# Kernel tuning notes

Hardware: AMD Instinct MI355X
Metric: run time of the kernel (lower is better)

Reference implementation:

```python
import jax, jax.numpy as jnp
import numpy as np

N_NODES = 100000
N_EDGES = 1600000
IN_FEAT = 128
EMBED = 64
N_LAYERS = 3
N_CENTROID = 100
N_CLASS = 10
EPS = 1e-12


def setup_inputs() -> dict:
    key = jax.random.key(0)
    ks = jax.random.split(key, 8)
    x = jax.random.normal(ks[0], (N_NODES, IN_FEAT), dtype=jnp.float32)
    edge_index = jax.random.randint(ks[1], (2, N_EDGES), 0, N_NODES, dtype=jnp.int64)
    W_embed = jax.random.normal(ks[2], (EMBED, IN_FEAT), dtype=jnp.float32) / np.sqrt(IN_FEAT)
    W_gcn = jax.random.normal(ks[3], (N_LAYERS, EMBED, EMBED), dtype=jnp.float32) / np.sqrt(EMBED)
    b_gcn = jnp.zeros((N_LAYERS, EMBED), dtype=jnp.float32)
    centroids = jax.random.normal(ks[4], (N_CENTROID, EMBED), dtype=jnp.float32)
    W_out = jax.random.normal(ks[5], (N_CLASS, N_CENTROID), dtype=jnp.float32) / np.sqrt(N_CENTROID)
    b_out = jnp.zeros((N_CLASS,), dtype=jnp.float32)
    return {"x": x, "edge_index": edge_index, "W_embed": W_embed, "W_gcn": W_gcn,
            "b_gcn": b_gcn, "centroids": centroids, "W_out": W_out, "b_out": b_out}


def _gcn_norm(edge_index, n, dtype):
    # add self loops, compute symmetric D^{-1/2}(A+I)D^{-1/2} edge weights
    loops = jnp.arange(n, dtype=edge_index.dtype)
    src = jnp.concatenate([edge_index[0], loops])
    dst = jnp.concatenate([edge_index[1], loops])
    deg = jax.ops.segment_sum(jnp.ones_like(dst, dtype=dtype), dst, num_segments=n)
    dinv = jax.lax.rsqrt(jnp.maximum(deg, 1.0))
    norm = dinv[src] * dinv[dst]  # [E+N]
    return src, dst, norm


def reference(x, edge_index, W_embed, W_gcn, b_gcn, centroids, W_out, b_out):
    n = x.shape[0]
    src, dst, norm = _gcn_norm(edge_index, n, x.dtype)
    # Euclidean manifold: log/exp are identity
    h = x @ W_embed.T  # [N, D]
    for l in range(W_gcn.shape[0]):
        hw = h @ W_gcn[l].T                                   # [N, D]
        msg = hw[src] * norm[:, None]                         # gather  [E+N, D]
        h = jax.ops.segment_sum(msg, dst, num_segments=n)     # scatter [N, D]
        h = jax.nn.relu(h + b_gcn[l])
    # centroid distances: ||h_i - c_k|| via expanded quadratic (avoids [N,K,D])
    h2 = jnp.sum(h * h, axis=-1, keepdims=True)               # [N, 1]
    c2 = jnp.sum(centroids * centroids, axis=-1)[None, :]     # [1, K]
    d2 = jnp.maximum(h2 + c2 - 2.0 * (h @ centroids.T), 0.0)  # [N, K]
    dist = jnp.sqrt(d2 + EPS)
    pooled = dist.mean(axis=0)                                # [K] graph pooling
    return pooled @ W_out.T + b_out                           # [num_class]
```

## Files before the change

### kernel.cpp

```cpp
#include <hip/hip_runtime.h>
#include <hip/hip_bf16.h>

typedef unsigned int uint32;
typedef float floatx2 __attribute__((ext_vector_type(2)));
typedef __attribute__((ext_vector_type(8))) short bf16x8;
typedef __attribute__((ext_vector_type(4))) float f32x4;

#define CHUNK 16384


__global__ __launch_bounds__(256) void k_bhist(const int* __restrict__ dst,
                                               int* __restrict__ bcnt,
                                               int E, int NBUCK, int NCH) {
    __shared__ int h[512];
    int c = blockIdx.x, tid = threadIdx.x;
    for (int i = tid; i < NBUCK; i += 256) h[i] = 0;
    __syncthreads();
    int base = c * CHUNK;
#pragma unroll
    for (int k = 0; k < CHUNK / 256; ++k) {
        int e = base + k * 256 + tid;
        if (e < E) atomicAdd(&h[dst[e] >> 8], 1);
    }
    __syncthreads();
    for (int i = tid; i < NBUCK; i += 256) bcnt[(size_t)i * NCH + c] = h[i];
}

__global__ __launch_bounds__(128) void k_bscan1(const int* __restrict__ bcnt,
                                                int* __restrict__ bofs,
                                                int* __restrict__ btot, int NCH) {
    __shared__ int tmp[128];
    int b = blockIdx.x, t = threadIdx.x;
    int v = (t < NCH) ? bcnt[(size_t)b * NCH + t] : 0;
    tmp[t] = v;
    __syncthreads();
    for (int off = 1; off < 128; off <<= 1) {
        int u = (t >= off) ? tmp[t - off] : 0;
        __syncthreads();
        tmp[t] += u;
        __syncthreads();
    }
    if (t < NCH) bofs[(size_t)b * NCH + t] = tmp[t] - v;
    if (t == 127) btot[b] = tmp[127];
}

__global__ __launch_bounds__(512) void k_bscan2(const int* __restrict__ btot,
                                                int* __restrict__ bbase, int nb) {
    __shared__ int tmp[512];
    int t = threadIdx.x;
    int v = (t < nb) ? btot[t] : 0;
    tmp[t] = v;
    __syncthreads();
    for (int off = 1; off < 512; off <<= 1) {
        int u = (t >= off) ? tmp[t - off] : 0;
        __syncthreads();
        tmp[t] += u;
        __syncthreads();
    }
    if (t < nb) bbase[t] = tmp[t] - v;
    if (t == nb - 1) bbase[nb] = tmp[t];
}

__global__ __launch_bounds__(256) void k_bscatter(const int* __restrict__ ei,
                                                  const int* __restrict__ bbase,
                                                  const int* __restrict__ bofs,
                                                  uint32* __restrict__ ebuf,
                                                  int E, int NBUCK, int NCH) {
    __shared__ int cur[512];
    int c = blockIdx.x, tid = threadIdx.x;
    for (int i = tid; i < NBUCK; i += 256)
        cur[i] = bbase[i] + bofs[(size_t)i * NCH + c];
    __syncthreads();
    int base = c * CHUNK;
#pragma unroll
    for (int k = 0; k < CHUNK / 256; ++k) {
        int e = base + k * 256 + tid;
        if (e < E) {
            int s = ei[e];
            int d = ei[E + e];
            int p = atomicAdd(&cur[d >> 8], 1);
            ebuf[p] = (uint32)s | ((uint32)(d & 255) << 20);
        }
    }
}

__global__ __launch_bounds__(256) void k_bsort(const uint32* __restrict__ ebuf,
                                               const int* __restrict__ bbase,
                                               int* __restrict__ ssrc,
                                               int2* __restrict__ rc,
                                               float* __restrict__ dinv, int N) {
    __shared__ int h[256];
    __shared__ int sc[256];
    __shared__ int cur[256];
    int b = blockIdx.x, tid = threadIdx.x;
    int beg = bbase[b], end = bbase[b + 1];
    h[tid] = 0;
    __syncthreads();
    for (int j = beg + tid; j < end; j += 256)
        atomicAdd(&h[(ebuf[j] >> 20) & 255], 1);
    __syncthreads();
    int v = h[tid];
    sc[tid] = v;
    __syncthreads();
    for (int off = 1; off < 256; off <<= 1) {
        int u = (tid >= off) ? sc[tid - off] : 0;
        __syncthreads();
        sc[tid] += u;
        __syncthreads();
    }
    int rowbase = beg + sc[tid] - v;
    cur[tid] = rowbase;
    int d = b * 256 + tid;
    if (d < N) {
        rc[d] = make_int2(rowbase, v);
        dinv[d] = rsqrtf((float)(v + 1));
    }
    __syncthreads();
    for (int j = beg + tid; j < end; j += 256) {
        uint32 w = ebuf[j];
        int p = atomicAdd(&cur[(w >> 20) & 255], 1);
        ssrc[p] = (int)(w & 0xFFFFFu);
    }
}


__device__ __forceinline__ short f2bf(float f) {
    __hip_bfloat16 b = __float2bfloat16(f);
    return __builtin_bit_cast(short, b);
}

__device__ __forceinline__ bf16x8 pack_bf16x8(float4 v0, float4 v1) {
    bf16x8 r;
    r[0] = f2bf(v0.x); r[1] = f2bf(v0.y); r[2] = f2bf(v0.z); r[3] = f2bf(v0.w);
    r[4] = f2bf(v1.x); r[5] = f2bf(v1.y); r[6] = f2bf(v1.z); r[7] = f2bf(v1.w);
    return r;
}


__global__ __launch_bounds__(256) void k_embed(const float* __restrict__ x,
                                               const float* __restrict__ We,
                                               float* __restrict__ h, int N) {
    int lane = threadIdx.x & 63;
    int w = threadIdx.x >> 6;
    int l15 = lane & 15;
    int lg = lane >> 4;

    bf16x8 B[4][4];
#pragma unroll
    for (int ct = 0; ct < 4; ++ct) {
        const float* wr = We + (size_t)(ct * 16 + l15) * 128 + lg * 8;
#pragma unroll
        for (int ks = 0; ks < 4; ++ks) {
            float4 v0 = *(const float4*)(wr + ks * 32);
            float4 v1 = *(const float4*)(wr + ks * 32 + 4);
            B[ct][ks] = pack_bf16x8(v0, v1);
        }
    }

    int rowbase = blockIdx.x * 256 + w * 64;

    f32x4 acc[4][4];
#pragma unroll
    for (int rt = 0; rt < 4; ++rt)
#pragma unroll
        for (int ct = 0; ct < 4; ++ct)
            acc[rt][ct] = (f32x4){0.f, 0.f, 0.f, 0.f};

#pragma unroll
    for (int ks = 0; ks < 4; ++ks) {
#pragma unroll
        for (int rt = 0; rt < 4; ++rt) {
            int row = rowbase + rt * 16 + l15;
            row = (row < N) ? row : (N - 1);
            const float* xr = x + (size_t)row * 128 + ks * 32 + lg * 8;
            float4 v0 = *(const float4*)xr;
            float4 v1 = *(const float4*)(xr + 4);
            bf16x8 a = pack_bf16x8(v0, v1);
#pragma unroll
            for (int ct = 0; ct < 4; ++ct)
                acc[rt][ct] = __builtin_amdgcn_mfma_f32_16x16x32_bf16(
                    a, B[ct][ks], acc[rt][ct], 0, 0, 0);
        }
    }

#pragma unroll
    for (int rt = 0; rt < 4; ++rt) {
        int row0 = rowbase + rt * 16 + lg * 4;
#pragma unroll
        for (int r = 0; r < 4; ++r) {
            int row = row0 + r;
            if (row < N) {
#pragma unroll
                for (int ct = 0; ct < 4; ++ct)
                    h[(size_t)row * 64 + ct * 16 + l15] = acc[rt][ct][r];
            }
        }
    }
}


__global__ __launch_bounds__(256) void k_gcn(const float* __restrict__ hin,
                                             const float* __restrict__ Wg,
                                             const float* __restrict__ bias_prev, int act,
                                             const float* __restrict__ dinv,
                                             uint32* __restrict__ tab, int N) {
    int lane = threadIdx.x & 63;
    int w = threadIdx.x >> 6;
    int l15 = lane & 15, lg = lane >> 4;

    bf16x8 A[4][2];
#pragma unroll
    for (int rt = 0; rt < 4; ++rt) {
        const float* wr = Wg + (size_t)(rt * 16 + l15) * 64 + lg * 8;
#pragma unroll
        for (int ks = 0; ks < 2; ++ks) {
            float4 v0 = *(const float4*)(wr + ks * 32);
            float4 v1 = *(const float4*)(wr + ks * 32 + 4);
            A[rt][ks] = pack_bf16x8(v0, v1);
        }
    }

    float bv[16];
#pragma unroll
    for (int ks = 0; ks < 2; ++ks) {
        float4 b0 = *(const float4*)(bias_prev + ks * 32 + lg * 8);
        float4 b1 = *(const float4*)(bias_prev + ks * 32 + lg * 8 + 4);
        bv[ks * 8 + 0] = b0.x; bv[ks * 8 + 1] = b0.y;
        bv[ks * 8 + 2] = b0.z; bv[ks * 8 + 3] = b0.w;
        bv[ks * 8 + 4] = b1.x; bv[ks * 8 + 5] = b1.y;
        bv[ks * 8 + 6] = b1.z; bv[ks * 8 + 7] = b1.w;
    }

    int nodebase = blockIdx.x * 256 + w * 64;

#pragma unroll
    for (int nt = 0; nt < 4; ++nt) {
        int node = nodebase + nt * 16 + l15;
        int nodec = (node < N) ? node : (N - 1);
        const float* hr = hin + ((size_t)nodec << 6) + lg * 8;

        bf16x8 Bf[2];
#pragma unroll
        for (int ks = 0; ks < 2; ++ks) {
            float4 v0 = *(const float4*)(hr + ks * 32);
            float4 v1 = *(const float4*)(hr + ks * 32 + 4);
            if (act) {
                v0.x = fmaxf(v0.x + bv[ks * 8 + 0], 0.f);
                v0.y = fmaxf(v0.y + bv[ks * 8 + 1], 0.f);
                v0.z = fmaxf(v0.z + bv[ks * 8 + 2], 0.f);
                v0.w = fmaxf(v0.w + bv[ks * 8 + 3], 0.f);
                v1.x = fmaxf(v1.x + bv[ks * 8 + 4], 0.f);
                v1.y = fmaxf(v1.y + bv[ks * 8 + 5], 0.f);
                v1.z = fmaxf(v1.z + bv[ks * 8 + 6], 0.f);
                v1.w = fmaxf(v1.w + bv[ks * 8 + 7], 0.f);
            }
            Bf[ks] = pack_bf16x8(v0, v1);
        }

        f32x4 acc[4];
#pragma unroll
        for (int rt = 0; rt < 4; ++rt) acc[rt] = (f32x4){0.f, 0.f, 0.f, 0.f};
#pragma unroll
        for (int ks = 0; ks < 2; ++ks)
#pragma unroll
            for (int rt = 0; rt < 4; ++rt)
                acc[rt] = __builtin_amdgcn_mfma_f32_16x16x32_bf16(
                    A[rt][ks], Bf[ks], acc[rt], 0, 0, 0);

        float s = dinv[nodec];
        if (node < N) {
#pragma unroll
            for (int rt = 0; rt < 4; ++rt) {
                int u = 0;
                u = __builtin_amdgcn_cvt_pk_fp8_f32(acc[rt][0] * s, acc[rt][1] * s, u, false);
                u = __builtin_amdgcn_cvt_pk_fp8_f32(acc[rt][2] * s, acc[rt][3] * s, u, true);
                tab[(size_t)node * 16 + rt * 4 + lg] = u;
            }
        }
    }
}


__global__ __launch_bounds__(256) void k_agg(const int2* __restrict__ rc,
                                             const int* __restrict__ ssrc,
                                             const float* __restrict__ dinv,
                                             const uint2* __restrict__ tab2,
                                             float* __restrict__ out, int N) {
    int lane = threadIdx.x & 63;
    int d = blockIdx.x * 4 + (threadIdx.x >> 6);
    if (d >= N) return;
    int q = lane & 7;
    int sub = lane >> 3;
    int l15 = lane & 15;
    int hi = lane & 48;

    floatx2 a01 = {0.f, 0.f}, a23 = {0.f, 0.f}, a45 = {0.f, 0.f}, a67 = {0.f, 0.f};
    auto accum = [&](uint2 v) {
        a01 += __builtin_amdgcn_cvt_pk_f32_fp8((int)v.x, false);
        a23 += __builtin_amdgcn_cvt_pk_f32_fp8((int)v.x, true);
        a45 += __builtin_amdgcn_cvt_pk_f32_fp8((int)v.y, false);
        a67 += __builtin_amdgcn_cvt_pk_f32_fp8((int)v.y, true);
    };

    {
        uint2 v = tab2[(size_t)d * 8 + q];
        if (sub == 0) accum(v);
    }

    int2 r = rc[d];
    int beg = __builtin_amdgcn_readfirstlane(r.x);
    int cnt = __builtin_amdgcn_readfirstlane(r.y);
    const int* srow = ssrc + beg;

    int j = 0;
    for (; j + 16 <= cnt; j += 16) {
        int ev = srow[j + l15];
        int t0 = __shfl(ev, hi | sub);
        int t1 = __shfl(ev, hi | 8 | sub);
        uint2 v0 = tab2[(size_t)t0 * 8 + q];
        uint2 v1 = tab2[(size_t)t1 * 8 + q];
        accum(v0);
        accum(v1);
    }
    int rem = cnt - j;
    if (rem) {
        int ev = srow[j + l15];
        int t0 = __shfl(ev, hi | sub);
        int t1 = __shfl(ev, hi | 8 | sub);
        t0 = (sub < rem) ? t0 : N;
        t1 = (sub + 8 < rem) ? t1 : N;
        uint2 v0 = tab2[(size_t)t0 * 8 + q];
        uint2 v1 = tab2[(size_t)t1 * 8 + q];
        accum(v0);
        accum(v1);
    }

    float a[8] = {a01.x, a01.y, a23.x, a23.y, a45.x, a45.y, a67.x, a67.y};
#pragma unroll
    for (int i = 0; i < 8; ++i) {
        a[i] += __shfl_xor(a[i], 8);
        a[i] += __shfl_xor(a[i], 16);
        a[i] += __shfl_xor(a[i], 32);
    }

    if (sub == 0) {
        float dd = dinv[d];
        float4* o4 = (float4*)out;
        o4[(size_t)d * 16 + 2 * q + 0] = make_float4(dd * a[0], dd * a[1], dd * a[2], dd * a[3]);
        o4[(size_t)d * 16 + 2 * q + 1] = make_float4(dd * a[4], dd * a[5], dd * a[6], dd * a[7]);
    }
}


__global__ void k_c2(const float* __restrict__ C, float* __restrict__ c2) {
    int k = threadIdx.x;
    if (k < 100) {
        float s = 0.f;
        for (int d = 0; d < 64; ++d) { float v = C[k * 64 + d]; s = fmaf(v, v, s); }
        c2[k] = s;
    }
}


__global__ __launch_bounds__(256) void k_cent(const float* __restrict__ hin,
                                              const float* __restrict__ b2,
                                              const float* __restrict__ C,
                                              const float* __restrict__ c2g,
                                              float* __restrict__ partials, int N) {
    __shared__ float pool4[4][112];
    __shared__ float h2_s[128];
    int tid = threadIdx.x;
    int lane = tid & 63, w = tid >> 6;
    int l15 = lane & 15, lg = lane >> 4;

    bf16x8 B[7][2];
#pragma unroll
    for (int ct = 0; ct < 7; ++ct) {
        int col = ct * 16 + l15;
#pragma unroll
        for (int ks = 0; ks < 2; ++ks) {
            float4 v0 = make_float4(0.f, 0.f, 0.f, 0.f);
            float4 v1 = make_float4(0.f, 0.f, 0.f, 0.f);
            if (col < 100) {
                const float* cr = C + (size_t)col * 64 + ks * 32 + lg * 8;
                v0 = *(const float4*)cr;
                v1 = *(const float4*)(cr + 4);
            }
            B[ct][ks] = pack_bf16x8(v0, v1);
        }
    }

    float bv[16];
#pragma unroll
    for (int ks = 0; ks < 2; ++ks) {
        float4 b0 = *(const float4*)(b2 + ks * 32 + lg * 8);
        float4 b1 = *(const float4*)(b2 + ks * 32 + lg * 8 + 4);
        bv[ks * 8 + 0] = b0.x; bv[ks * 8 + 1] = b0.y;
        bv[ks * 8 + 2] = b0.z; bv[ks * 8 + 3] = b0.w;
        bv[ks * 8 + 4] = b1.x; bv[ks * 8 + 5] = b1.y;
        bv[ks * 8 + 6] = b1.z; bv[ks * 8 + 7] = b1.w;
    }

    int rowbase = blockIdx.x * 128 + w * 32;

    f32x4 acc[2][7];
#pragma unroll
    for (int rt = 0; rt < 2; ++rt)
#pragma unroll
        for (int ct = 0; ct < 7; ++ct)
            acc[rt][ct] = (f32x4){0.f, 0.f, 0.f, 0.f};

#pragma unroll
    for (int rt = 0; rt < 2; ++rt) {
        int row = rowbase + rt * 16 + l15;
        int rowc = (row < N) ? row : (N - 1);
        const float* hr = hin + ((size_t)rowc << 6);
        float hp[16];
        float h2p = 0.f;
#pragma unroll
        for (int ks = 0; ks < 2; ++ks) {
            float4 v0 = *(const float4*)(hr + ks * 32 + lg * 8);
            float4 v1 = *(const float4*)(hr + ks * 32 + lg * 8 + 4);
            float t0 = fmaxf(v0.x + bv[ks * 8 + 0], 0.f);
            float t1 = fmaxf(v0.y + bv[ks * 8 + 1], 0.f);
            float t2 = fmaxf(v0.z + bv[ks * 8 + 2], 0.f);
            float t3 = fmaxf(v0.w + bv[ks * 8 + 3], 0.f);
            float t4 = fmaxf(v1.x + bv[ks * 8 + 4], 0.f);
            float t5 = fmaxf(v1.y + bv[ks * 8 + 5], 0.f);
            float t6 = fmaxf(v1.z + bv[ks * 8 + 6], 0.f);
            float t7 = fmaxf(v1.w + bv[ks * 8 + 7], 0.f);
            hp[ks * 8 + 0] = t0; hp[ks * 8 + 1] = t1;
            hp[ks * 8 + 2] = t2; hp[ks * 8 + 3] = t3;
            hp[ks * 8 + 4] = t4; hp[ks * 8 + 5] = t5;
            hp[ks * 8 + 6] = t6; hp[ks * 8 + 7] = t7;
            h2p = fmaf(t0, t0, h2p); h2p = fmaf(t1, t1, h2p);
            h2p = fmaf(t2, t2, h2p); h2p = fmaf(t3, t3, h2p);
            h2p = fmaf(t4, t4, h2p); h2p = fmaf(t5, t5, h2p);
            h2p = fmaf(t6, t6, h2p); h2p = fmaf(t7, t7, h2p);
        }
        h2p += __shfl_xor(h2p, 16);
        h2p += __shfl_xor(h2p, 32);
        if (lg == 0) h2_s[w * 32 + rt * 16 + l15] = h2p;

#pragma unroll
        for (int ks = 0; ks < 2; ++ks) {
            bf16x8 a;
#pragma unroll
            for (int j = 0; j < 8; ++j) a[j] = f2bf(hp[ks * 8 + j]);
#pragma unroll
            for (int ct = 0; ct < 7; ++ct)
                acc[rt][ct] = __builtin_amdgcn_mfma_f32_16x16x32_bf16(
                    a, B[ct][ks], acc[rt][ct], 0, 0, 0);
        }
    }

    float S[7] = {0.f, 0.f, 0.f, 0.f, 0.f, 0.f, 0.f};
#pragma unroll
    for (int rt = 0; rt < 2; ++rt) {
#pragma unroll
        for (int r = 0; r < 4; ++r) {
            int row = rowbase + rt * 16 + lg * 4 + r;
            float h2v = h2_s[w * 32 + rt * 16 + lg * 4 + r];
            bool rv = row < N;
#pragma unroll
            for (int ct = 0; ct < 7; ++ct) {
                int col = ct * 16 + l15;
                float c2v = (col < 100) ? c2g[col] : 0.f;
                float G = acc[rt][ct][r];
                float d2 = fmaxf(h2v + c2v - 2.f * G, 0.f);
                float xx = d2 + 1e-12f;
                float dist = xx * __frsqrt_rn(xx);
                S[ct] += (rv && col < 100) ? dist : 0.f;
            }
        }
    }
#pragma unroll
    for (int ct = 0; ct < 7; ++ct) {
        float s = S[ct];
        s += __shfl_xor(s, 16);
        s += __shfl_xor(s, 32);
        if (lg == 0) pool4[w][ct * 16 + l15] = s;
    }
    __syncthreads();
    if (tid < 112) {
        float s = pool4[0][tid] + pool4[1][tid] + pool4[2][tid] + pool4[3][tid];
        partials[(size_t)blockIdx.x * 128 + tid] = s;
    }
}


__global__ __launch_bounds__(1024) void k_out(const float* __restrict__ partials, int nb,
                                              const float* __restrict__ Wout,
                                              const float* __restrict__ bout,
                                              float* __restrict__ out, float invN) {
    __shared__ float ps[8][112];
    int t = threadIdx.x & 127, g = threadIdx.x >> 7;
    if (t < 112) {
        float s0 = 0.f, s1 = 0.f, s2 = 0.f, s3 = 0.f;
        float s4 = 0.f, s5 = 0.f, s6 = 0.f, s7 = 0.f;
        int b = g;
        for (; b + 56 < nb; b += 64) {
            s0 += partials[(size_t)(b     ) * 128 + t];
            s1 += partials[(size_t)(b +  8) * 128 + t];
            s2 += partials[(size_t)(b + 16) * 128 + t];
            s3 += partials[(size_t)(b + 24) * 128 + t];
            s4 += partials[(size_t)(b + 32) * 128 + t];
            s5 += partials[(size_t)(b + 40) * 128 + t];
            s6 += partials[(size_t)(b + 48) * 128 + t];
            s7 += partials[(size_t)(b + 56) * 128 + t];
        }
        for (; b < nb; b += 8) s0 += partials[(size_t)b * 128 + t];
        ps[g][t] = ((s0 + s1) + (s2 + s3)) + ((s4 + s5) + (s6 + s7));
    }
    __syncthreads();
    if (threadIdx.x < 10) {
        int tt = threadIdx.x;
        float s = 0.f;
        for (int k = 0; k < 100; ++k) {
            float p = ps[0][k] + ps[1][k] + ps[2][k] + ps[3][k]
                    + ps[4][k] + ps[5][k] + ps[6][k] + ps[7][k];
            s = fmaf(p, Wout[tt * 100 + k], s);
        }
        out[tt] = s * invN + bout[tt];
    }
}


extern "C" void kernel_launch(void* const* d_in, const int* in_sizes, int n_in,
                              void* d_out, int out_size, void* d_ws, size_t ws_size,
                              hipStream_t stream) {
    const float* x    = (const float*)d_in[0];
    const int*   ei   = (const int*)d_in[1];
    const float* We   = (const float*)d_in[2];
    const float* Wg   = (const float*)d_in[3];
    const float* bg   = (const float*)d_in[4];
    const float* C    = (const float*)d_in[5];
    const float* Wout = (const float*)d_in[6];
    const float* bout = (const float*)d_in[7];
    float*       out  = (float*)d_out;

    const int N = in_sizes[0] / 128;
    const int E = in_sizes[1] / 2;
    const int NBUCK = (N + 255) >> 8;
    const int NCH = (E + CHUNK - 1) / CHUNK;
    const int NBC = (N + 127) / 128;

    char* ws = (char*)d_ws;
    size_t off = 0;
    auto alloc = [&](size_t bytes) { void* p = ws + off; off += (bytes + 511) & ~(size_t)511; return p; };
    float*  dinv   = (float*)alloc((size_t)N * 4);
    int2*   rc     = (int2*) alloc((size_t)N * 8);
    int*    bcnt   = (int*)  alloc((size_t)NBUCK * NCH * 4);
    int*    bofs   = (int*)  alloc((size_t)NBUCK * NCH * 4);
    int*    btot   = (int*)  alloc((size_t)NBUCK * 4);
    int*    bbase  = (int*)  alloc((size_t)(NBUCK + 1) * 4);
    uint32* ebuf   = (uint32*)alloc((size_t)E * 4);
    int*    ssrc   = (int*)  alloc((size_t)(E + 16) * 4);
    float*  hA     = (float*)alloc((size_t)N * 64 * 4);
    uint32* tab    = (uint32*)alloc((size_t)(N + 1) * 64);
    float*  c2     = (float*)alloc(512);
    float*  partials = (float*)alloc((size_t)NBC * 128 * 4);

    hipMemsetAsync(tab + (size_t)N * 16, 0, 64, stream);

    k_bhist<<<NCH, 256, 0, stream>>>(ei + E, bcnt, E, NBUCK, NCH);
    k_bscan1<<<NBUCK, 128, 0, stream>>>(bcnt, bofs, btot, NCH);
    k_bscan2<<<1, 512, 0, stream>>>(btot, bbase, NBUCK);
    k_bscatter<<<NCH, 256, 0, stream>>>(ei, bbase, bofs, ebuf, E, NBUCK, NCH);
    k_bsort<<<NBUCK, 256, 0, stream>>>(ebuf, bbase, ssrc, rc, dinv, N);
    k_c2<<<1, 128, 0, stream>>>(C, c2);

    k_embed<<<(N + 255) / 256, 256, 0, stream>>>(x, We, hA, N);

    for (int l = 0; l < 3; ++l) {
        const float* bias_prev = (l == 0) ? bg : (bg + (l - 1) * 64);
        int act = (l == 0) ? 0 : 1;
        k_gcn<<<(N + 255) / 256, 256, 0, stream>>>(hA, Wg + (size_t)l * 64 * 64,
                                                   bias_prev, act, dinv, tab, N);
        k_agg<<<(N + 3) / 4, 256, 0, stream>>>(rc, ssrc, dinv,
                                               (const uint2*)tab, hA, N);
    }

    k_cent<<<NBC, 256, 0, stream>>>(hA, bg + 2 * 64, C, c2, partials, N);

    k_out<<<1, 1024, 0, stream>>>(partials, NBC, Wout, bout, out, 1.0f / (float)N);
}
```

Baseline: 383.9 us.

## Split FP8 feature table into two halves and aggregate 16 nodes per wave

```diff
diff --git a/kernel.cpp b/kernel.cpp
--- a/kernel.cpp
+++ b/kernel.cpp
@@ -203,7 +203,8 @@
                                              const float* __restrict__ Wg,
                                              const float* __restrict__ bias_prev, int act,
                                              const float* __restrict__ dinv,
-                                             uint32* __restrict__ tab, int N) {
+                                             uint32* __restrict__ tab0,
+                                             uint32* __restrict__ tab1, int N) {
     int lane = threadIdx.x & 63;
     int w = threadIdx.x >> 6;
     int l15 = lane & 15, lg = lane >> 4;
@@ -274,7 +275,8 @@
                 int u = 0;
                 u = __builtin_amdgcn_cvt_pk_fp8_f32(acc[rt][0] * s, acc[rt][1] * s, u, false);
                 u = __builtin_amdgcn_cvt_pk_fp8_f32(acc[rt][2] * s, acc[rt][3] * s, u, true);
-                tab[(size_t)node * 16 + rt * 4 + lg] = u;
+                uint32* tp = (rt < 2) ? tab0 : tab1;
+                tp[(size_t)node * 8 + (rt & 1) * 4 + lg] = u;
             }
         }
     }
@@ -284,15 +286,21 @@
 __global__ __launch_bounds__(256) void k_agg(const int2* __restrict__ rc,
                                              const int* __restrict__ ssrc,
                                              const float* __restrict__ dinv,
-                                             const uint2* __restrict__ tab2,
-                                             float* __restrict__ out, int N) {
+                                             const uint2* __restrict__ tabh,
+                                             float* __restrict__ outh,
+                                             int N, int E) {
     int lane = threadIdx.x & 63;
-    int d = blockIdx.x * 4 + (threadIdx.x >> 6);
-    if (d >= N) return;
-    int q = lane & 7;
-    int sub = lane >> 3;
-    int l15 = lane & 15;
-    int hi = lane & 48;
+    int wid = threadIdx.x >> 6;
+    int q = lane & 3;
+    int g = lane >> 2;
+    int dbase = (blockIdx.x * 4 + wid) * 16;
+    if (dbase >= N) return;
+
+    int2 r = rc[min(dbase + (lane & 15), N - 1)];
+    int beg = __shfl(r.x, g);
+    int deg = __shfl(r.y, g);
+    int dg = dbase + g;
+    if (dg >= N) deg = 0;
 
     floatx2 a01 = {0.f, 0.f}, a23 = {0.f, 0.f}, a45 = {0.f, 0.f}, a67 = {0.f, 0.f};
     auto accum = [&](uint2 v) {
@@ -303,51 +311,35 @@
     };
 
     {
-        uint2 v = tab2[(size_t)d * 8 + q];
-        if (sub == 0) accum(v);
-    }
-
-    int2 r = rc[d];
-    int beg = __builtin_amdgcn_readfirstlane(r.x);
-    int cnt = __builtin_amdgcn_readfirstlane(r.y);
-    const int* srow = ssrc + beg;
-
-    int j = 0;
-    for (; j + 16 <= cnt; j += 16) {
-        int ev = srow[j + l15];
-        int t0 = __shfl(ev, hi | sub);
-        int t1 = __shfl(ev, hi | 8 | sub);
-        uint2 v0 = tab2[(size_t)t0 * 8 + q];
-        uint2 v1 = tab2[(size_t)t1 * 8 + q];
-        accum(v0);
-        accum(v1);
-    }
-    int rem = cnt - j;
-    if (rem) {
-        int ev = srow[j + l15];
-        int t0 = __shfl(ev, hi | sub);
-        int t1 = __shfl(ev, hi | 8 | sub);
-        t0 = (sub < rem) ? t0 : N;
-        t1 = (sub + 8 < rem) ? t1 : N;
-        uint2 v0 = tab2[(size_t)t0 * 8 + q];
-        uint2 v1 = tab2[(size_t)t1 * 8 + q];
-        accum(v0);
-        accum(v1);
-    }
-
-    float a[8] = {a01.x, a01.y, a23.x, a23.y, a45.x, a45.y, a67.x, a67.y};
-#pragma unroll
-    for (int i = 0; i < 8; ++i) {
-        a[i] += __shfl_xor(a[i], 8);
-        a[i] += __shfl_xor(a[i], 16);
-        a[i] += __shfl_xor(a[i], 32);
-    }
-
-    if (sub == 0) {
-        float dd = dinv[d];
-        float4* o4 = (float4*)out;
-        o4[(size_t)d * 16 + 2 * q + 0] = make_float4(dd * a[0], dd * a[1], dd * a[2], dd * a[3]);
-        o4[(size_t)d * 16 + 2 * q + 1] = make_float4(dd * a[4], dd * a[5], dd * a[6], dd * a[7]);
+        int t = (dg < N) ? dg : N;
+        accum(tabh[(size_t)t * 4 + q]);
+    }
+
+    int m = deg;
+    m = max(m, __shfl_xor(m, 4));
+    m = max(m, __shfl_xor(m, 8));
+    m = max(m, __shfl_xor(m, 16));
+    m = max(m, __shfl_xor(m, 32));
+    int maxd = __builtin_amdgcn_readfirstlane(m);
+
+    int ev = 0;
+    for (int j = 0; j < maxd; ++j) {
+        if ((j & 3) == 0) {
+            int idx = beg + j + q;
+            ev = ssrc[idx < E ? idx : 0];
+        }
+        int t = __shfl(ev, (lane & 60) | (j & 3));
+        t = (j < deg) ? t : N;
+        accum(tabh[(size_t)t * 4 + q]);
+    }
+
+    if (dg < N) {
+        float dd = dinv[dg];
+        float* orow = outh + (size_t)dg * 64 + q * 8;
+        f32x4 o0 = {dd * a01.x, dd * a01.y, dd * a23.x, dd * a23.y};
+        f32x4 o1 = {dd * a45.x, dd * a45.y, dd * a67.x, dd * a67.y};
+        __builtin_nontemporal_store(o0, (f32x4*)orow);
+        __builtin_nontemporal_store(o1, (f32x4*)(orow + 4));
     }
 }
 
@@ -544,6 +536,7 @@
     const int NBUCK = (N + 255) >> 8;
     const int NCH = (E + CHUNK - 1) / CHUNK;
     const int NBC = (N + 127) / 128;
+    const int NBA = (N + 63) / 64;
 
     char* ws = (char*)d_ws;
     size_t off = 0;
@@ -555,13 +548,15 @@
     int*    btot   = (int*)  alloc((size_t)NBUCK * 4);
     int*    bbase  = (int*)  alloc((size_t)(NBUCK + 1) * 4);
     uint32* ebuf   = (uint32*)alloc((size_t)E * 4);
-    int*    ssrc   = (int*)  alloc((size_t)(E + 16) * 4);
+    int*    ssrc   = (int*)  alloc((size_t)(E + 64) * 4);
     float*  hA     = (float*)alloc((size_t)N * 64 * 4);
-    uint32* tab    = (uint32*)alloc((size_t)(N + 1) * 64);
+    uint32* tab0   = (uint32*)alloc((size_t)(N + 1) * 32);
+    uint32* tab1   = (uint32*)alloc((size_t)(N + 1) * 32);
     float*  c2     = (float*)alloc(512);
     float*  partials = (float*)alloc((size_t)NBC * 128 * 4);
 
-    hipMemsetAsync(tab + (size_t)N * 16, 0, 64, stream);
+    hipMemsetAsync(tab0 + (size_t)N * 8, 0, 32, stream);
+    hipMemsetAsync(tab1 + (size_t)N * 8, 0, 32, stream);
 
     k_bhist<<<NCH, 256, 0, stream>>>(ei + E, bcnt, E, NBUCK, NCH);
     k_bscan1<<<NBUCK, 128, 0, stream>>>(bcnt, bofs, btot, NCH);
@@ -576,9 +571,9 @@
         const float* bias_prev = (l == 0) ? bg : (bg + (l - 1) * 64);
         int act = (l == 0) ? 0 : 1;
         k_gcn<<<(N + 255) / 256, 256, 0, stream>>>(hA, Wg + (size_t)l * 64 * 64,
-                                                   bias_prev, act, dinv, tab, N);
-        k_agg<<<(N + 3) / 4, 256, 0, stream>>>(rc, ssrc, dinv,
-                                               (const uint2*)tab, hA, N);
+                                                   bias_prev, act, dinv, tab0, tab1, N);
+        k_agg<<<NBA, 256, 0, stream>>>(rc, ssrc, dinv, (const uint2*)tab0, hA, N, E);
+        k_agg<<<NBA, 256, 0, stream>>>(rc, ssrc, dinv, (const uint2*)tab1, hA + 32, N, E);
     }
 
     k_cent<<<NBC, 256, 0, stream>>>(hA, bg + 2 * 64, C, c2, partials, N);
```

New measurement: 373.5 us. 2.7% less time.
